# Kernel optimization log

Hardware: AMD Instinct MI355X
Metric: run time of the kernel (lower is better)

Reference implementation:

```python
import jax, jax.numpy as jnp
import numpy as np

B, N, K = 8, 1024, 20


def _w(key, o, i):
    return jax.random.normal(key, (o, i), dtype=jnp.float32) * (1.0 / np.sqrt(i))


def setup_inputs() -> dict:
    key = jax.random.key(0)
    ks = iter(jax.random.split(key, 64))
    d = {"inputs": jax.random.normal(next(ks), (B, 3, N, 1), dtype=jnp.float32)}
    shapes = {
        "he_w1": (32, 12), "he_w2": (64, 32), "hn_w1": (32, 67), "hn_w2": (64, 32),
        "b1e_w1": (48, 192), "b1e_w2": (128, 48), "b1n_w1": (48, 192), "b1n_w2": (128, 48),
        "b2e_w1": (96, 384), "b2e_w2": (192, 96), "b2n_w1": (96, 320), "b2n_w2": (192, 96),
        "f_w": (512, 384), "p1_w": (256, 512), "p2_w": (128, 256), "p3_w": (40, 128),
    }
    for name, (o, i) in shapes.items():
        d[name] = _w(next(ks), o, i)
        d[name.replace("_w", "_b")] = jnp.zeros((o,), dtype=jnp.float32)
    return d


def _conv(x, w, b):
    # BasicConv with norm=None: 1x1 Conv2d + bias. x: [B,C,N,k]
    return jnp.einsum('bcnk,oc->bonk', x, w) + b[None, :, None, None]


def _conv_relu(x, w, b):
    return jax.nn.relu(_conv(x, w, b))


def _gather(x, idx):
    # batched_index_select: x [B,C,N,1], idx [B,N,k] -> [B,C,N,k]
    b, c, n, _ = x.shape
    k = idx.shape[-1]
    out = jnp.take_along_axis(x[:, :, :, 0], idx.reshape(b, 1, n * k), axis=2)
    return out.reshape(b, c, n, k)


def _knn(x, k):
    # DenseKnnGraph: x [B,C,N,1] -> (nn_idx, center_idx), each [B,N,k]
    xt = jnp.transpose(x[:, :, :, 0], (0, 2, 1))  # [B,N,C]
    sq = jnp.sum(xt * xt, axis=-1, keepdims=True)
    dist = sq - 2.0 * jnp.einsum('bnc,bmc->bnm', xt, xt) + jnp.transpose(sq, (0, 2, 1))
    _, nn_idx = jax.lax.top_k(-dist, k)
    center = jnp.broadcast_to(jnp.arange(x.shape[2])[None, :, None], nn_idx.shape)
    return nn_idx, center


def _mp(nf, e_ij, nn_idx, center, ew1, eb1, ew2, eb2, nw1, nb1, nw2, nb2):
    # MessagePassing block (Kearnes et al. style)
    h_i = _gather(nf, center)  # [B,Cin,N,k]
    h_j = _gather(nf, nn_idx)
    e_p = _conv_relu(_conv_relu(jnp.concatenate([e_ij, h_i, h_j], axis=1), ew1, eb1), ew2, eb2)
    m = jnp.broadcast_to(jnp.sum(e_p, axis=3, keepdims=True),
                         e_p.shape[:3] + (h_i.shape[-1],))
    h_p = _conv_relu(_conv_relu(jnp.concatenate([h_i, m], axis=1), nw1, nb1), nw2, nb2)
    return h_p[:, :, :, 0:1], e_p


def reference(inputs, he_w1, he_b1, he_w2, he_b2, hn_w1, hn_b1, hn_w2, hn_b2,
              b1e_w1, b1e_b1, b1e_w2, b1e_b2, b1n_w1, b1n_b1, b1n_w2, b1n_b2,
              b2e_w1, b2e_b1, b2e_w2, b2e_b2, b2n_w1, b2n_b1, b2n_w2, b2n_b2,
              f_w, f_b, p1_w, p1_b, p2_w, p2_b, p3_w, p3_b):
    nn_idx, center = _knn(inputs[:, 0:3], K)
    # initial edge features: (h_i, h_i - h_j) on xyz-KNN graph
    gh_i = _gather(inputs, center)
    gh_j = _gather(inputs, nn_idx)
    e_ij = jnp.concatenate([gh_i, gh_i - gh_j], axis=1)  # [B, 2*in, N, k]
    h1, e1 = _mp(inputs, e_ij, nn_idx, center, he_w1, he_b1, he_w2, he_b2, hn_w1, hn_b1, hn_w2, hn_b2)
    h2, e2 = _mp(h1, e1, nn_idx, center, b1e_w1, b1e_b1, b1e_w2, b1e_b2, b1n_w1, b1n_b1, b1n_w2, b1n_b2)
    h3, e3 = _mp(h2, e2, nn_idx, center, b2e_w1, b2e_b1, b2e_w2, b2e_b2, b2n_w1, b2n_b1, b2n_w2, b2n_b2)
    feats = jnp.concatenate([h1, h2, h3], axis=1)  # [B, 384, N, 1]
    fus = _conv_relu(feats, f_w, f_b)  # [B, 512, N, 1]
    pooled = jnp.max(fus, axis=(2, 3), keepdims=True)  # max_pool2d over [N,1]
    # prediction head (dropout = identity at inference)
    pred = _conv(_conv_relu(_conv_relu(pooled, p1_w, p1_b), p2_w, p2_b), p3_w, p3_b)
    return pred[:, :, :, 0], inputs  # (logits [B,n_classes,1], edge_features)
```

## Files before the change

kernel.cpp:

```cpp
#include <hip/hip_runtime.h>

#define BDIM 8
#define NDIM 1024
#define KNN 20

typedef unsigned short u16;
typedef float f32x4 __attribute__((ext_vector_type(4)));
typedef short short8 __attribute__((ext_vector_type(8)));
typedef unsigned short ushort8 __attribute__((ext_vector_type(8)));

__device__ inline u16 f2bf(float f) {
  unsigned u = __float_as_uint(f);
  unsigned r = (u + 0x7fffu + ((u >> 16) & 1u)) >> 16;
  return (u16)r;
}
__device__ inline float bf2f(u16 v) {
  return __uint_as_float(((unsigned)v) << 16);
}

__global__ __launch_bounds__(256) void knn_wcvt(
    const float* __restrict__ x, int* __restrict__ nn,
    const float* __restrict__ w1_3, const float* __restrict__ w2_3,
    const float* __restrict__ w1_2, const float* __restrict__ w2_2,
    const float* __restrict__ hn_w1, const float* __restrict__ f_w,
    const float* __restrict__ he_w1, const float* __restrict__ he_w2,
    u16* __restrict__ w1b3e, u16* __restrict__ wpq3, u16* __restrict__ w2b3,
    u16* __restrict__ w1b2e, u16* __restrict__ wpq2, u16* __restrict__ w2b2,
    float* __restrict__ w1p1, u16* __restrict__ fwb,
    u16* __restrict__ w1b1, u16* __restrict__ w2b1, int* __restrict__ pooled) {
  const int tid = threadIdx.x;
  if (blockIdx.x >= BDIM * 256) {
    const int idx = (blockIdx.x - BDIM * 256) * 256 + tid;
    if (idx < 512 * 384) fwb[idx] = f2bf(f_w[idx]);
    if (idx < 96 * 128) {
      int oc = idx >> 7, c = idx & 127;
      w1b3e[idx] = f2bf(w1_3[oc * 384 + c]);
    }
    if (idx < 192 * 128) {
      int n = idx >> 7, c = idx & 127;
      wpq3[idx] = f2bf(n < 96 ? w1_3[n * 384 + 128 + c]
                              : w1_3[(n - 96) * 384 + 256 + c]);
    }
    if (idx < 192 * 96) w2b3[idx] = f2bf(w2_3[idx]);
    if (idx < 48 * 64) {
      int oc = idx >> 6, c = idx & 63;
      w1b2e[idx] = f2bf(w1_2[oc * 192 + c]);
    }
    if (idx < 96 * 64) {
      int n = idx >> 6, c = idx & 63;
      wpq2[idx] = f2bf(n < 48 ? w1_2[n * 192 + 64 + c]
                              : w1_2[(n - 48) * 192 + 128 + c]);
    }
    if (idx < 128 * 64) {
      int oc = idx >> 6, i = idx & 63;
      w2b2[idx] = (i < 48) ? f2bf(w2_2[oc * 48 + i]) : (u16)0;
    }
    if (idx < 32 * 68) {
      int oc = idx / 68, c = idx - oc * 68;
      w1p1[idx] = (c < 67) ? hn_w1[oc * 67 + c] : 0.0f;
    }
    if (idx < 32 * 32) {
      int oc = idx >> 5, c = idx & 31;
      w1b1[idx] = (c < 12) ? f2bf(he_w1[oc * 12 + c]) : (u16)0;
    }
    if (idx < 64 * 32) w2b1[idx] = f2bf(he_w2[idx]);
    if (idx < BDIM * 512) pooled[idx] = 0;
    return;
  }
  {
#pragma clang fp contract(off)
    __shared__ float xs0[NDIM], xs1[NDIM], xs2[NDIM], sq[NDIM];
    const int lane = tid & 63;
    const int w = tid >> 6;
    const int b = blockIdx.x >> 8;
    const int n = ((blockIdx.x & 255) << 2) + w;
    for (int i = tid; i < NDIM; i += 256) {
      float a0 = x[(b * 3 + 0) * NDIM + i];
      float a1 = x[(b * 3 + 1) * NDIM + i];
      float a2 = x[(b * 3 + 2) * NDIM + i];
      xs0[i] = a0; xs1[i] = a1; xs2[i] = a2;
      sq[i] = (a0 * a0 + a1 * a1) + a2 * a2;
    }
    __syncthreads();
    const float xn0 = xs0[n], xn1 = xs1[n], xn2 = xs2[n], sqn = sq[n];
    float dl[16];
#pragma unroll
    for (int t = 0; t < 16; ++t) {
      int m = t * 64 + lane;
      float dot = (xn0 * xs0[m] + xn1 * xs1[m]) + xn2 * xs2[m];
      dl[t] = (sqn - 2.0f * dot) + sq[m];
    }
    int* nnrow = &nn[(b * NDIM + n) * KNN];
    for (int r = 0; r < KNN; ++r) {
      float bd = dl[0];
      int bt = 0;
#pragma unroll
      for (int t = 1; t < 16; ++t) {
        if (dl[t] < bd) { bd = dl[t]; bt = t; }
      }
      int bi = bt * 64 + lane;
#pragma unroll
      for (int off = 1; off < 64; off <<= 1) {
        float pd = __shfl_xor(bd, off);
        int pi = __shfl_xor(bi, off);
        if (pd < bd || (pd == bd && pi < bi)) { bd = pd; bi = pi; }
      }
      if (lane == 0) nnrow[r] = bi;
      if ((bi & 63) == lane) {
        int wt = bi >> 6;
#pragma unroll
        for (int t = 0; t < 16; ++t) {
          if (t == wt) dl[t] = 3.4e38f;
        }
      }
    }
  }
}

template <int PTS, int CE, int CMID, int COUT, bool WRITE_E, bool FIRST>
__global__ __launch_bounds__(256) void edge_mfma(
    const u16* __restrict__ eprev, const float* __restrict__ finput,
    const int* __restrict__ nnb, const u16* __restrict__ w1b,
    const float* __restrict__ b1v, const u16* __restrict__ w2b,
    const float* __restrict__ b2v, const u16* __restrict__ pq,
    u16* __restrict__ eout, float* __restrict__ mout) {
  constexpr int K2 = (CMID + 31) & ~31;
  constexpr int NPQ = 2 * CMID;
  constexpr int MT = PTS * KNN;
  constexpr int MTL = MT / 16;
  constexpr int XPB = CE + 8;
  constexpr int QYP = K2 + 8;
  __shared__ u16 Xs[MT * XPB];
  __shared__ u16 QY[MT * QYP];
  __shared__ float pld[FIRST ? 8 : PTS * CMID];
  const int tid = threadIdx.x;
  const int lane = tid & 63;
  const int wv = tid >> 6;
  const int q = lane >> 4;
  const int bn0 = blockIdx.x * PTS;
  const int b = bn0 >> 10;
  if constexpr (FIRST) {
    for (int idx = tid; idx < MT * (CE / 8); idx += 256) {
      int p = idx / (CE / 8), kc = idx - p * (CE / 8);
      int k0 = kc * 8;
      int bn = bn0 + p / KNN;
      int n = bn & (NDIM - 1);
      int j = nnb[(size_t)bn0 * KNN + p];
      ushort8 r;
#pragma unroll
      for (int t = 0; t < 8; ++t) {
        int c = k0 + t;
        float v = 0.0f;
        if (c < 3) v = finput[(b * 3 + c) * NDIM + n];
        else if (c < 6)
          v = finput[(b * 3 + c - 3) * NDIM + n] -
              finput[(b * 3 + c - 3) * NDIM + j];
        else if (c < 9) v = finput[(b * 3 + c - 6) * NDIM + n];
        else if (c < 12) v = finput[(b * 3 + c - 9) * NDIM + j];
        r[t] = f2bf(v);
      }
      *(ushort8*)&Xs[p * XPB + k0] = r;
    }
  } else {
    constexpr int KC = CE / 8;
    for (int ch = tid; ch < MT * KC; ch += 256) {
      int p = ch / KC, kc = ch - p * KC;
      int k0 = kc * 8;
      *(uint4*)&Xs[p * XPB + k0] =
          *(const uint4*)&eprev[((size_t)blockIdx.x * MT + p) * CE + k0];
    }
    constexpr int QC = CMID / 8;
    for (int i = tid; i < MT * QC; i += 256) {
      int p = i / QC, c8 = (i - p * QC) * 8;
      int j = nnb[(size_t)bn0 * KNN + p];
      *(uint4*)&QY[p * QYP + c8] =
          *(const uint4*)&pq[((size_t)(b << 10) + j) * NPQ + CMID + c8];
    }
    if constexpr (K2 != CMID) {
      constexpr int PC = (K2 - CMID) / 8;
      for (int i = tid; i < MT * PC; i += 256) {
        int p = i / PC, c8 = CMID + (i - p * PC) * 8;
        uint4 z = {0, 0, 0, 0};
        *(uint4*)&QY[p * QYP + c8] = z;
      }
    }
    for (int i = tid; i < PTS * CMID; i += 256) {
      int pt = i / CMID, c = i - pt * CMID;
      pld[i] = bf2f(pq[(size_t)(bn0 + pt) * NPQ + c]) + b1v[c];
    }
  }
  __syncthreads();
  {
    constexpr int NT1 = CMID / 16;
    constexpr int J1 = MTL * NT1;
    constexpr int KS1 = CE / 32;
    for (int job = wv; job < J1; job += 4) {
      int mt = job / NT1, nt = job - mt * NT1;
      int row = mt * 16 + (lane & 15);
      int ncol = nt * 16 + (lane & 15);
      int kb = q * 8;
      f32x4 acc = {0.f, 0.f, 0.f, 0.f};
      const u16* ap = &Xs[row * XPB + kb];
      const u16* bp = &w1b[(size_t)ncol * CE + kb];
#pragma unroll
      for (int ks = 0; ks < KS1; ++ks) {
        short8 a = *(const short8*)(ap + ks * 32);
        short8 bb = *(const short8*)(bp + ks * 32);
        acc = __builtin_amdgcn_mfma_f32_16x16x32_bf16(a, bb, acc, 0, 0, 0);
      }
      int m0 = mt * 16 + q * 4;
      if constexpr (FIRST) {
        float bias = b1v[ncol];
#pragma unroll
        for (int r = 0; r < 4; ++r) {
          float yv = fmaxf(acc[r] + bias, 0.0f);
          QY[(m0 + r) * QYP + ncol] = f2bf(yv);
        }
      } else {
        int pt = m0 / KNN;
        float padd = pld[pt * CMID + ncol];
#pragma unroll
        for (int r = 0; r < 4; ++r) {
          int m = m0 + r;
          float qadd = bf2f(QY[m * QYP + ncol]);
          float yv = fmaxf(acc[r] + padd + qadd, 0.0f);
          QY[m * QYP + ncol] = f2bf(yv);
        }
      }
    }
  }
  __syncthreads();
  {
    constexpr int NT2 = COUT / 16;
    constexpr int KS2 = K2 / 32;
    for (int nt = wv; nt < NT2; nt += 4) {
      int ncol = nt * 16 + (lane & 15);
      int kb = q * 8;
      short8 bfrag[KS2];
      const u16* bp = &w2b[(size_t)ncol * K2 + kb];
#pragma unroll
      for (int ks = 0; ks < KS2; ++ks)
        bfrag[ks] = *(const short8*)(bp + ks * 32);
      float bias = b2v[ncol];
      float s[PTS];
#pragma unroll
      for (int pt = 0; pt < PTS; ++pt) s[pt] = 0.0f;
#pragma unroll
      for (int mt = 0; mt < MTL; ++mt) {
        f32x4 acc = {0.f, 0.f, 0.f, 0.f};
        const u16* ap = &QY[(mt * 16 + (lane & 15)) * QYP + kb];
#pragma unroll
        for (int ks = 0; ks < KS2; ++ks) {
          short8 a = *(const short8*)(ap + ks * 32);
          acc = __builtin_amdgcn_mfma_f32_16x16x32_bf16(a, bfrag[ks], acc, 0, 0, 0);
        }
        int m0 = mt * 16 + q * 4;
        float part = 0.0f;
#pragma unroll
        for (int r = 0; r < 4; ++r) {
          float yv = fmaxf(acc[r] + bias, 0.0f);
          if (WRITE_E)
            eout[((size_t)blockIdx.x * MT + m0 + r) * COUT + ncol] = f2bf(yv);
          part += yv;
        }
        int ptA = (4 * mt) / 5;
        int ptB = (4 * mt + 3) / 5;
        int qb = 5 * ptB - 4 * mt;
#pragma unroll
        for (int pt2 = 0; pt2 < PTS; ++pt2) {
          if (pt2 == ptA && ptA == ptB) s[pt2] += part;
          else if (pt2 == ptA) s[pt2] += (q < qb) ? part : 0.0f;
          else if (pt2 == ptB) s[pt2] += (q < qb) ? 0.0f : part;
        }
      }
#pragma unroll
      for (int pt = 0; pt < PTS; ++pt) {
        float sv = s[pt];
        sv += __shfl_xor(sv, 16);
        sv += __shfl_xor(sv, 32);
        if (lane < 16)
          mout[(size_t)(bn0 + pt) * COUT + nt * 16 + lane] = sv;
      }
    }
  }
}

template <int TP, int CH, int CM, int CINP, int CMID, int COUT, int NPQ, bool FIRSTH>
__global__ __launch_bounds__(256) void node_conv(
    const float* __restrict__ h, const float* __restrict__ inputs,
    const float* __restrict__ mbuf, const float* __restrict__ w1p,
    const float* __restrict__ b1v, const float* __restrict__ w2,
    const float* __restrict__ b2v, float* __restrict__ hout,
    const u16* __restrict__ wpq, u16* __restrict__ pq) {
  constexpr int CIN = CH + CM;
  constexpr int XP = CINP + 4;
  constexpr int Y1P = CMID + 4;
  constexpr int PG = TP / 4;
  constexpr int HP = COUT + 8;
  __shared__ float Xs[TP * XP];
  __shared__ float Y1s[TP * Y1P];
  __shared__ u16 Hb[(NPQ > 0) ? TP * HP : 8];
  const int tid = threadIdx.x;
  const int bn0 = blockIdx.x * TP;
  if constexpr (FIRSTH) {
    for (int idx = tid; idx < TP * CIN; idx += 256) {
      int p = idx / CIN, c = idx - p * CIN;
      int bn = bn0 + p;
      int b = bn >> 10, n = bn & (NDIM - 1);
      Xs[p * XP + c] = (c < CH) ? inputs[(b * 3 + c) * NDIM + n]
                                : mbuf[(size_t)bn * CM + (c - CH)];
    }
    if constexpr (CINP > CIN) {
      constexpr int PAD = CINP - CIN;
      for (int idx = tid; idx < TP * PAD; idx += 256) {
        int p = idx / PAD, c = CIN + idx % PAD;
        Xs[p * XP + c] = 0.0f;
      }
    }
  } else {
    constexpr int C4 = CIN / 4;
    for (int idx = tid; idx < TP * C4; idx += 256) {
      int p = idx / C4, c = (idx - p * C4) * 4;
      int bn = bn0 + p;
      float4 v = (c < CH) ? *(const float4*)&h[(size_t)bn * CH + c]
                          : *(const float4*)&mbuf[(size_t)bn * CM + (c - CH)];
      *(float4*)&Xs[p * XP + c] = v;
    }
  }
  __syncthreads();
  {
    constexpr int NT1 = PG * (CMID / 4);
    for (int t = tid; t < NT1; t += 256) {
      int pg = t % PG, og = t / PG;
      float acc[4][4];
#pragma unroll
      for (int j = 0; j < 4; ++j) {
        float bj = b1v[og * 4 + j];
#pragma unroll
        for (int i = 0; i < 4; ++i) acc[i][j] = bj;
      }
      for (int cin = 0; cin < CINP; cin += 4) {
        float4 xr[4], wr[4];
#pragma unroll
        for (int i = 0; i < 4; ++i)
          xr[i] = *(const float4*)&Xs[(pg * 4 + i) * XP + cin];
#pragma unroll
        for (int j = 0; j < 4; ++j)
          wr[j] = *(const float4*)&w1p[(size_t)(og * 4 + j) * CINP + cin];
#pragma unroll
        for (int i = 0; i < 4; ++i)
#pragma unroll
          for (int j = 0; j < 4; ++j) {
            acc[i][j] += xr[i].x * wr[j].x;
            acc[i][j] += xr[i].y * wr[j].y;
            acc[i][j] += xr[i].z * wr[j].z;
            acc[i][j] += xr[i].w * wr[j].w;
          }
      }
#pragma unroll
      for (int i = 0; i < 4; ++i)
#pragma unroll
        for (int j = 0; j < 4; ++j)
          Y1s[(pg * 4 + i) * Y1P + og * 4 + j] = fmaxf(acc[i][j], 0.0f);
    }
  }
  __syncthreads();
  {
    constexpr int NT2 = PG * (COUT / 4);
    for (int t = tid; t < NT2; t += 256) {
      int pg = t % PG, og = t / PG;
      float acc[4][4];
#pragma unroll
      for (int j = 0; j < 4; ++j) {
        float bj = b2v[og * 4 + j];
#pragma unroll
        for (int i = 0; i < 4; ++i) acc[i][j] = bj;
      }
      for (int cin = 0; cin < CMID; cin += 4) {
        float4 xr[4], wr[4];
#pragma unroll
        for (int i = 0; i < 4; ++i)
          xr[i] = *(const float4*)&Y1s[(pg * 4 + i) * Y1P + cin];
#pragma unroll
        for (int j = 0; j < 4; ++j)
          wr[j] = *(const float4*)&w2[(size_t)(og * 4 + j) * CMID + cin];
#pragma unroll
        for (int i = 0; i < 4; ++i)
#pragma unroll
          for (int j = 0; j < 4; ++j) {
            acc[i][j] += xr[i].x * wr[j].x;
            acc[i][j] += xr[i].y * wr[j].y;
            acc[i][j] += xr[i].z * wr[j].z;
            acc[i][j] += xr[i].w * wr[j].w;
          }
      }
#pragma unroll
      for (int i = 0; i < 4; ++i) {
        int bn = bn0 + pg * 4 + i;
#pragma unroll
        for (int j = 0; j < 4; ++j) {
          float v = fmaxf(acc[i][j], 0.0f);
          hout[(size_t)bn * COUT + og * 4 + j] = v;
          if constexpr (NPQ > 0) Hb[(pg * 4 + i) * HP + og * 4 + j] = f2bf(v);
        }
      }
    }
  }
  if constexpr (NPQ > 0) {
    __syncthreads();
    const int lane = tid & 63;
    const int wv = tid >> 6;
    constexpr int NT = NPQ / 16;
    constexpr int JOBS = (TP / 16) * NT;
    constexpr int KS = COUT / 32;
    for (int job = wv; job < JOBS; job += 4) {
      int mt = job / NT, nt = job - mt * NT;
      int row = mt * 16 + (lane & 15);
      int ncol = nt * 16 + (lane & 15);
      int kb = (lane >> 4) * 8;
      f32x4 acc = {0.f, 0.f, 0.f, 0.f};
      const u16* ap = &Hb[row * HP + kb];
      const u16* bp = &wpq[(size_t)ncol * COUT + kb];
#pragma unroll
      for (int ks = 0; ks < KS; ++ks) {
        short8 a = *(const short8*)(ap + ks * 32);
        short8 bb = *(const short8*)(bp + ks * 32);
        acc = __builtin_amdgcn_mfma_f32_16x16x32_bf16(a, bb, acc, 0, 0, 0);
      }
      int m0 = mt * 16 + (lane >> 4) * 4;
#pragma unroll
      for (int r = 0; r < 4; ++r)
        pq[(size_t)(bn0 + m0 + r) * NPQ + ncol] = f2bf(acc[r]);
    }
  }
}

__global__ __launch_bounds__(256) void fuse_pool_mfma(
    const float* __restrict__ h1, const float* __restrict__ h2,
    const float* __restrict__ h3, const u16* __restrict__ fwb,
    const float* __restrict__ fb, int* __restrict__ pooled) {
  constexpr int CIN = 384, COUT = 512, TP = 32;
  constexpr int XPB = CIN + 8;
  __shared__ u16 Xs[TP * XPB];
  __shared__ int pmax[COUT];
  const int tid = threadIdx.x;
  const int lane = tid & 63;
  const int wv = tid >> 6;
  const int bn0 = blockIdx.x * TP;
  const int b = bn0 >> 10;
  for (int i = tid; i < COUT; i += 256) pmax[i] = 0;
  constexpr int KC = CIN / 8;
  for (int ch = tid; ch < TP * KC; ch += 256) {
    int p = ch / KC, kc = ch - p * KC;
    int k0 = kc * 8;
    int bn = bn0 + p;
    const float* src;
    if (k0 < 64) src = &h1[(size_t)bn * 64 + k0];
    else if (k0 < 192) src = &h2[(size_t)bn * 128 + (k0 - 64)];
    else src = &h3[(size_t)bn * 192 + (k0 - 192)];
    float4 f0 = *(const float4*)src;
    float4 f1 = *(const float4*)(src + 4);
    ushort8 r;
    r[0] = f2bf(f0.x); r[1] = f2bf(f0.y); r[2] = f2bf(f0.z); r[3] = f2bf(f0.w);
    r[4] = f2bf(f1.x); r[5] = f2bf(f1.y); r[6] = f2bf(f1.z); r[7] = f2bf(f1.w);
    *(ushort8*)&Xs[p * XPB + k0] = r;
  }
  __syncthreads();
  constexpr int NT = COUT / 16;
  constexpr int JOBS = (TP / 16) * NT;
  constexpr int KS = CIN / 32;
  for (int job = wv; job < JOBS; job += 4) {
    int mt = job / NT, nt = job - mt * NT;
    int row = mt * 16 + (lane & 15);
    int ncol = nt * 16 + (lane & 15);
    int kb = (lane >> 4) * 8;
    f32x4 acc = {0.f, 0.f, 0.f, 0.f};
    const u16* ap = &Xs[row * XPB + kb];
    const u16* bp = &fwb[(size_t)ncol * CIN + kb];
#pragma unroll
    for (int ks = 0; ks < KS; ++ks) {
      short8 a = *(const short8*)(ap + ks * 32);
      short8 bb = *(const short8*)(bp + ks * 32);
      acc = __builtin_amdgcn_mfma_f32_16x16x32_bf16(a, bb, acc, 0, 0, 0);
    }
    float bias = fb[ncol];
    float v = fmaxf(fmaxf(acc[0], acc[1]), fmaxf(acc[2], acc[3]));
    v = fmaxf(v + bias, 0.0f);
    v = fmaxf(v, __shfl_xor(v, 16));
    v = fmaxf(v, __shfl_xor(v, 32));
    if (lane < 16) atomicMax(&pmax[ncol], __float_as_int(v));
  }
  __syncthreads();
  for (int i = tid; i < COUT; i += 256)
    atomicMax(&pooled[b * COUT + i], pmax[i]);
}

__global__ __launch_bounds__(256) void head_kernel(
    const int* __restrict__ pooledi, const float* __restrict__ p1w,
    const float* __restrict__ p1b, const float* __restrict__ p2w,
    const float* __restrict__ p2b, const float* __restrict__ p3w,
    const float* __restrict__ p3b, const float* __restrict__ inputs,
    float* __restrict__ out) {
  const int tid = threadIdx.x;
  if (blockIdx.x >= BDIM) {
    int idx = (blockIdx.x - BDIM) * 256 + tid;
    if (idx < (BDIM * 3 * NDIM) / 4) {
      const float4* src = (const float4*)inputs;
      float4* dst = (float4*)(out + BDIM * 40);
      dst[idx] = src[idx];
    }
    return;
  }
  __shared__ float xs[512], y1[256], y2[128];
  const int b = blockIdx.x;
  for (int i = tid; i < 512; i += 256) xs[i] = __int_as_float(pooledi[b * 512 + i]);
  __syncthreads();
  {
    float acc = p1b[tid];
    for (int c = 0; c < 512; ++c) acc += xs[c] * p1w[tid * 512 + c];
    y1[tid] = fmaxf(acc, 0.0f);
  }
  __syncthreads();
  if (tid < 128) {
    float acc = p2b[tid];
    for (int c = 0; c < 256; ++c) acc += y1[c] * p2w[tid * 256 + c];
    y2[tid] = fmaxf(acc, 0.0f);
  }
  __syncthreads();
  if (tid < 40) {
    float acc = p3b[tid];
    for (int c = 0; c < 128; ++c) acc += y2[c] * p3w[tid * 128 + c];
    out[b * 40 + tid] = acc;
  }
}

extern "C" void kernel_launch(void* const* d_in, const int* in_sizes, int n_in,
                              void* d_out, int out_size, void* d_ws,
                              size_t ws_size, hipStream_t stream) {
  const float* inputs = (const float*)d_in[0];
  const float* he_w1 = (const float*)d_in[1];
  const float* he_b1 = (const float*)d_in[2];
  const float* he_w2 = (const float*)d_in[3];
  const float* he_b2 = (const float*)d_in[4];
  const float* hn_w1 = (const float*)d_in[5];
  const float* hn_b1 = (const float*)d_in[6];
  const float* hn_w2 = (const float*)d_in[7];
  const float* hn_b2 = (const float*)d_in[8];
  const float* b1e_w1 = (const float*)d_in[9];
  const float* b1e_b1 = (const float*)d_in[10];
  const float* b1e_w2 = (const float*)d_in[11];
  const float* b1e_b2 = (const float*)d_in[12];
  const float* b1n_w1 = (const float*)d_in[13];
  const float* b1n_b1 = (const float*)d_in[14];
  const float* b1n_w2 = (const float*)d_in[15];
  const float* b1n_b2 = (const float*)d_in[16];
  const float* b2e_w1 = (const float*)d_in[17];
  const float* b2e_b1 = (const float*)d_in[18];
  const float* b2e_w2 = (const float*)d_in[19];
  const float* b2e_b2 = (const float*)d_in[20];
  const float* b2n_w1 = (const float*)d_in[21];
  const float* b2n_b1 = (const float*)d_in[22];
  const float* b2n_w2 = (const float*)d_in[23];
  const float* b2n_b2 = (const float*)d_in[24];
  const float* f_w = (const float*)d_in[25];
  const float* f_b = (const float*)d_in[26];
  const float* p1_w = (const float*)d_in[27];
  const float* p1_b = (const float*)d_in[28];
  const float* p2_w = (const float*)d_in[29];
  const float* p2_b = (const float*)d_in[30];
  const float* p3_w = (const float*)d_in[31];
  const float* p3_b = (const float*)d_in[32];
  float* out = (float*)d_out;

  char* ws = (char*)d_ws;
  size_t off = 0;
  auto alloc = [&](size_t bytes) {
    void* p = ws + off;
    off += (bytes + 255) & ~(size_t)255;
    return p;
  };
  int* nn = (int*)alloc((size_t)BDIM * NDIM * KNN * 4);
  float* m1 = (float*)alloc((size_t)BDIM * NDIM * 64 * 4);
  float* h1 = (float*)alloc((size_t)BDIM * NDIM * 64 * 4);
  u16* e1 = (u16*)alloc((size_t)BDIM * NDIM * KNN * 64 * 2);
  float* m2 = (float*)alloc((size_t)BDIM * NDIM * 128 * 4);
  float* h2 = (float*)alloc((size_t)BDIM * NDIM * 128 * 4);
  u16* e2 = (u16*)alloc((size_t)BDIM * NDIM * KNN * 128 * 2);
  float* m3 = (float*)alloc((size_t)BDIM * NDIM * 192 * 4);
  float* h3 = (float*)alloc((size_t)BDIM * NDIM * 192 * 4);
  u16* pq2 = (u16*)alloc((size_t)BDIM * NDIM * 96 * 2);
  u16* pq3 = (u16*)alloc((size_t)BDIM * NDIM * 192 * 2);
  int* pooled = (int*)alloc((size_t)BDIM * 512 * 4);
  u16* w1b3e = (u16*)alloc((size_t)96 * 128 * 2);
  u16* wpq3 = (u16*)alloc((size_t)192 * 128 * 2);
  u16* w2b3 = (u16*)alloc((size_t)192 * 96 * 2);
  u16* w1b2e = (u16*)alloc((size_t)48 * 64 * 2);
  u16* wpq2 = (u16*)alloc((size_t)96 * 64 * 2);
  u16* w2b2 = (u16*)alloc((size_t)128 * 64 * 2);
  float* w1p1 = (float*)alloc((size_t)32 * 68 * 4);
  u16* fwb = (u16*)alloc((size_t)512 * 384 * 2);
  u16* w1b1 = (u16*)alloc((size_t)32 * 32 * 2);
  u16* w2b1 = (u16*)alloc((size_t)64 * 32 * 2);

  knn_wcvt<<<BDIM * 256 + 768, 256, 0, stream>>>(
      inputs, nn, b2e_w1, b2e_w2, b1e_w1, b1e_w2, hn_w1, f_w, he_w1, he_w2,
      w1b3e, wpq3, w2b3, w1b2e, wpq2, w2b2, w1p1, fwb, w1b1, w2b1, pooled);

  edge_mfma<4, 32, 32, 64, true, true><<<BDIM * NDIM / 4, 256, 0, stream>>>(
      nullptr, inputs, nn, w1b1, he_b1, w2b1, he_b2, nullptr, e1, m1);
  node_conv<64, 3, 64, 68, 32, 64, 96, true><<<BDIM * NDIM / 64, 256, 0, stream>>>(
      nullptr, inputs, m1, w1p1, hn_b1, hn_w2, hn_b2, h1, wpq2, pq2);

  edge_mfma<4, 64, 48, 128, true, false><<<BDIM * NDIM / 4, 256, 0, stream>>>(
      e1, nullptr, nn, w1b2e, b1e_b1, w2b2, b1e_b2, pq2, e2, m2);
  node_conv<32, 64, 128, 192, 48, 128, 192, false><<<BDIM * NDIM / 32, 256, 0, stream>>>(
      h1, nullptr, m2, b1n_w1, b1n_b1, b1n_w2, b1n_b2, h2, wpq3, pq3);

  edge_mfma<4, 128, 96, 192, false, false><<<BDIM * NDIM / 4, 256, 0, stream>>>(
      e2, nullptr, nn, w1b3e, b2e_b1, w2b3, b2e_b2, pq3, nullptr, m3);
  node_conv<16, 128, 192, 320, 96, 192, 0, false><<<BDIM * NDIM / 16, 256, 0, stream>>>(
      h2, nullptr, m3, b2n_w1, b2n_b1, b2n_w2, b2n_b2, h3, nullptr, nullptr);

  fuse_pool_mfma<<<BDIM * NDIM / 32, 256, 0, stream>>>(h1, h2, h3, fwb, f_b,
                                                       pooled);
  head_kernel<<<BDIM + 24, 256, 0, stream>>>(pooled, p1_w, p1_b, p2_w, p2_b,
                                             p3_w, p3_b, inputs, out);
}
```

Before: 247.6 us.

## Fuse third-block node convolution into the last edge MFMA kernel

The third block's node MLP now runs at the end of the edge kernel, using the per-point message sums kept in shared memory instead of writing m3 to global memory and launching a separate node_conv. The node weights are converted to bf16 in the setup kernel and the two node layers are computed with bf16 MFMA on a 16-row tile, of which only 4 rows are valid. This removes one kernel launch and the m3 round trip through global memory. In exchange it computes padded rows that are thrown away, reuses the edge shared memory, and lowers node-layer precision from fp32 to bf16.

```diff
diff --git a/kernel.cpp b/kernel.cpp
--- a/kernel.cpp
+++ b/kernel.cpp
@@ -24,10 +24,12 @@
     const float* __restrict__ w1_2, const float* __restrict__ w2_2,
     const float* __restrict__ hn_w1, const float* __restrict__ f_w,
     const float* __restrict__ he_w1, const float* __restrict__ he_w2,
+    const float* __restrict__ bn_w1, const float* __restrict__ bn_w2,
     u16* __restrict__ w1b3e, u16* __restrict__ wpq3, u16* __restrict__ w2b3,
     u16* __restrict__ w1b2e, u16* __restrict__ wpq2, u16* __restrict__ w2b2,
     float* __restrict__ w1p1, u16* __restrict__ fwb,
-    u16* __restrict__ w1b1, u16* __restrict__ w2b1, int* __restrict__ pooled) {
+    u16* __restrict__ w1b1, u16* __restrict__ w2b1,
+    u16* __restrict__ wn1b, u16* __restrict__ wn2b, int* __restrict__ pooled) {
   const int tid = threadIdx.x;
   if (blockIdx.x >= BDIM * 256) {
     const int idx = (blockIdx.x - BDIM * 256) * 256 + tid;
@@ -64,6 +66,8 @@
       w1b1[idx] = (c < 12) ? f2bf(he_w1[oc * 12 + c]) : (u16)0;
     }
     if (idx < 64 * 32) w2b1[idx] = f2bf(he_w2[idx]);
+    if (idx < 96 * 320) wn1b[idx] = f2bf(bn_w1[idx]);
+    if (idx < 192 * 96) wn2b[idx] = f2bf(bn_w2[idx]);
     if (idx < BDIM * 512) pooled[idx] = 0;
     return;
   }
@@ -117,21 +121,28 @@
   }
 }
 
-template <int PTS, int CE, int CMID, int COUT, bool WRITE_E, bool FIRST>
+template <int PTS, int CE, int CMID, int COUT, bool WRITE_E, bool FIRST, bool FUSE_N>
 __global__ __launch_bounds__(256) void edge_mfma(
     const u16* __restrict__ eprev, const float* __restrict__ finput,
     const int* __restrict__ nnb, const u16* __restrict__ w1b,
     const float* __restrict__ b1v, const u16* __restrict__ w2b,
     const float* __restrict__ b2v, const u16* __restrict__ pq,
-    u16* __restrict__ eout, float* __restrict__ mout) {
+    u16* __restrict__ eout, float* __restrict__ mout,
+    const float* __restrict__ hprev, const u16* __restrict__ wn1b,
+    const float* __restrict__ bn1v, const u16* __restrict__ wn2b,
+    const float* __restrict__ bn2v, float* __restrict__ h3out) {
   constexpr int K2 = (CMID + 31) & ~31;
   constexpr int NPQ = 2 * CMID;
   constexpr int MT = PTS * KNN;
   constexpr int MTL = MT / 16;
   constexpr int XPB = CE + 8;
   constexpr int QYP = K2 + 8;
-  __shared__ u16 Xs[MT * XPB];
-  __shared__ u16 QY[MT * QYP];
+  __shared__ __align__(16) char smem[MT * XPB * 2 + MT * QYP * 2];
+  u16* Xs = (u16*)smem;
+  u16* QY = (u16*)(smem + (size_t)MT * XPB * 2);
+  float* msum = (float*)smem;
+  u16* Xn = (u16*)(smem + 3072);
+  u16* Y1n = (u16*)(smem + 3072 + 16 * 328 * 2);
   __shared__ float pld[FIRST ? 8 : PTS * CMID];
   const int tid = threadIdx.x;
   const int lane = tid & 63;
@@ -278,8 +289,78 @@
         float sv = s[pt];
         sv += __shfl_xor(sv, 16);
         sv += __shfl_xor(sv, 32);
-        if (lane < 16)
-          mout[(size_t)(bn0 + pt) * COUT + nt * 16 + lane] = sv;
+        if (lane < 16) {
+          if constexpr (FUSE_N)
+            msum[pt * COUT + nt * 16 + lane] = sv;
+          else
+            mout[(size_t)(bn0 + pt) * COUT + nt * 16 + lane] = sv;
+        }
+      }
+    }
+  }
+  if constexpr (FUSE_N) {
+    constexpr int XNP = 328;
+    constexpr int Y1NP = 104;
+    __syncthreads();
+    for (int i = tid; i < 4 * 41; i += 256) {
+      int p = i / 41, kc = i - p * 41;
+      int k0 = kc * 8;
+      ushort8 r;
+      if (kc < 16) {
+        const float* src = &hprev[(size_t)(bn0 + p) * 128 + k0];
+        float4 f0 = *(const float4*)src;
+        float4 f1 = *(const float4*)(src + 4);
+        r[0] = f2bf(f0.x); r[1] = f2bf(f0.y); r[2] = f2bf(f0.z); r[3] = f2bf(f0.w);
+        r[4] = f2bf(f1.x); r[5] = f2bf(f1.y); r[6] = f2bf(f1.z); r[7] = f2bf(f1.w);
+      } else if (kc < 40) {
+        const float* src = &msum[p * 192 + (k0 - 128)];
+#pragma unroll
+        for (int t = 0; t < 8; ++t) r[t] = f2bf(src[t]);
+      } else {
+#pragma unroll
+        for (int t = 0; t < 8; ++t) r[t] = 0;
+      }
+      *(ushort8*)&Xn[p * XNP + k0] = r;
+    }
+    __syncthreads();
+    for (int nt = wv; nt < 6; nt += 4) {
+      int ncol = nt * 16 + (lane & 15);
+      int kb = q * 8;
+      f32x4 acc = {0.f, 0.f, 0.f, 0.f};
+      const u16* ap = &Xn[(lane & 15) * XNP + kb];
+      const u16* bp = &wn1b[(size_t)ncol * 320 + kb];
+#pragma unroll
+      for (int ks = 0; ks < 10; ++ks) {
+        short8 a = *(const short8*)(ap + ks * 32);
+        short8 bb = *(const short8*)(bp + ks * 32);
+        acc = __builtin_amdgcn_mfma_f32_16x16x32_bf16(a, bb, acc, 0, 0, 0);
+      }
+      float bias = bn1v[ncol];
+      int m0 = q * 4;
+#pragma unroll
+      for (int r = 0; r < 4; ++r)
+        Y1n[(m0 + r) * Y1NP + ncol] = f2bf(fmaxf(acc[r] + bias, 0.0f));
+    }
+    __syncthreads();
+    for (int nt = wv; nt < 12; nt += 4) {
+      int ncol = nt * 16 + (lane & 15);
+      int kb = q * 8;
+      f32x4 acc = {0.f, 0.f, 0.f, 0.f};
+      const u16* ap = &Y1n[(lane & 15) * Y1NP + kb];
+      const u16* bp = &wn2b[(size_t)ncol * 96 + kb];
+#pragma unroll
+      for (int ks = 0; ks < 3; ++ks) {
+        short8 a = *(const short8*)(ap + ks * 32);
+        short8 bb = *(const short8*)(bp + ks * 32);
+        acc = __builtin_amdgcn_mfma_f32_16x16x32_bf16(a, bb, acc, 0, 0, 0);
+      }
+      float bias = bn2v[ncol];
+      int m0 = q * 4;
+#pragma unroll
+      for (int r = 0; r < 4; ++r) {
+        int m = m0 + r;
+        if (m < 4)
+          h3out[(size_t)(bn0 + m) * 192 + ncol] = fmaxf(acc[r] + bias, 0.0f);
       }
     }
   }
@@ -586,7 +667,6 @@
   float* m2 = (float*)alloc((size_t)BDIM * NDIM * 128 * 4);
   float* h2 = (float*)alloc((size_t)BDIM * NDIM * 128 * 4);
   u16* e2 = (u16*)alloc((size_t)BDIM * NDIM * KNN * 128 * 2);
-  float* m3 = (float*)alloc((size_t)BDIM * NDIM * 192 * 4);
   float* h3 = (float*)alloc((size_t)BDIM * NDIM * 192 * 4);
   u16* pq2 = (u16*)alloc((size_t)BDIM * NDIM * 96 * 2);
   u16* pq3 = (u16*)alloc((size_t)BDIM * NDIM * 192 * 2);
@@ -601,25 +681,29 @@
   u16* fwb = (u16*)alloc((size_t)512 * 384 * 2);
   u16* w1b1 = (u16*)alloc((size_t)32 * 32 * 2);
   u16* w2b1 = (u16*)alloc((size_t)64 * 32 * 2);
+  u16* wn1b = (u16*)alloc((size_t)96 * 320 * 2);
+  u16* wn2b = (u16*)alloc((size_t)192 * 96 * 2);
 
   knn_wcvt<<<BDIM * 256 + 768, 256, 0, stream>>>(
       inputs, nn, b2e_w1, b2e_w2, b1e_w1, b1e_w2, hn_w1, f_w, he_w1, he_w2,
-      w1b3e, wpq3, w2b3, w1b2e, wpq2, w2b2, w1p1, fwb, w1b1, w2b1, pooled);
-
-  edge_mfma<4, 32, 32, 64, true, true><<<BDIM * NDIM / 4, 256, 0, stream>>>(
-      nullptr, inputs, nn, w1b1, he_b1, w2b1, he_b2, nullptr, e1, m1);
+      b2n_w1, b2n_w2, w1b3e, wpq3, w2b3, w1b2e, wpq2, w2b2, w1p1, fwb, w1b1,
+      w2b1, wn1b, wn2b, pooled);
+
+  edge_mfma<4, 32, 32, 64, true, true, false><<<BDIM * NDIM / 4, 256, 0, stream>>>(
+      nullptr, inputs, nn, w1b1, he_b1, w2b1, he_b2, nullptr, e1, m1, nullptr,
+      nullptr, nullptr, nullptr, nullptr, nullptr);
   node_conv<64, 3, 64, 68, 32, 64, 96, true><<<BDIM * NDIM / 64, 256, 0, stream>>>(
       nullptr, inputs, m1, w1p1, hn_b1, hn_w2, hn_b2, h1, wpq2, pq2);
 
-  edge_mfma<4, 64, 48, 128, true, false><<<BDIM * NDIM / 4, 256, 0, stream>>>(
-      e1, nullptr, nn, w1b2e, b1e_b1, w2b2, b1e_b2, pq2, e2, m2);
+  edge_mfma<4, 64, 48, 128, true, false, false><<<BDIM * NDIM / 4, 256, 0, stream>>>(
+      e1, nullptr, nn, w1b2e, b1e_b1, w2b2, b1e_b2, pq2, e2, m2, nullptr,
+      nullptr, nullptr, nullptr, nullptr, nullptr);
   node_conv<32, 64, 128, 192, 48, 128, 192, false><<<BDIM * NDIM / 32, 256, 0, stream>>>(
       h1, nullptr, m2, b1n_w1, b1n_b1, b1n_w2, b1n_b2, h2, wpq3, pq3);
 
-  edge_mfma<4, 128, 96, 192, false, false><<<BDIM * NDIM / 4, 256, 0, stream>>>(
-      e2, nullptr, nn, w1b3e, b2e_b1, w2b3, b2e_b2, pq3, nullptr, m3);
-  node_conv<16, 128, 192, 320, 96, 192, 0, false><<<BDIM * NDIM / 16, 256, 0, stream>>>(
-      h2, nullptr, m3, b2n_w1, b2n_b1, b2n_w2, b2n_b2, h3, nullptr, nullptr);
+  edge_mfma<4, 128, 96, 192, false, false, true><<<BDIM * NDIM / 4, 256, 0, stream>>>(
+      e2, nullptr, nn, w1b3e, b2e_b1, w2b3, b2e_b2, pq3, nullptr, nullptr, h2,
+      wn1b, b2n_b1, wn2b, b2n_b2, h3);
 
   fuse_pool_mfma<<<BDIM * NDIM / 32, 256, 0, stream>>>(h1, h2, h3, fwb, f_b,
                                                        pooled);
```

Result: faster. 238.2 us (-3.8%).
